# Kernel tuning notes

Hardware: AMD Instinct MI355X
Metric: run time of the kernel (lower is better)

The kernel has to match this reference:

```python
import jax, jax.numpy as jnp
import numpy as np

TOP_K = 2
EPS = 1e-10


def setup_inputs() -> dict:
    key = jax.random.key(0)
    k1, k2, k3, k4 = jax.random.split(key, 4)
    B, S, H, E = 4, 2048, 1024, 8
    tokens = jax.random.normal(k1, (B, S, H), dtype=jnp.float32)
    router_w = jax.random.normal(k2, (E, H), dtype=jnp.float32) * (1.0 / np.sqrt(H))
    router_b = jax.random.normal(k3, (E,), dtype=jnp.float32) * 0.01
    expert_weights = jax.random.normal(k4, (E, H, H), dtype=jnp.float32) * (1.0 / np.sqrt(H))
    return {"tokens": tokens, "router_w": router_w, "router_b": router_b,
            "expert_weights": expert_weights}


def reference(tokens, router_w, router_b, expert_weights):
    B, S, H = tokens.shape
    E = expert_weights.shape[0]
    # Router (torch Linear: x @ W^T + b)
    logits = jnp.einsum('bsh,eh->bse', tokens, router_w) + router_b  # [B,S,E]
    probs = jax.nn.softmax(logits, axis=-1)
    top_p, top_i = jax.lax.top_k(probs, TOP_K)            # [B,S,K]
    w = top_p / (jnp.sum(top_p, axis=-1, keepdims=True) + EPS)  # normalized weights

    x = tokens.reshape(-1, H)                              # [N,H]
    idx = top_i.reshape(-1, TOP_K)                         # [N,K]
    wf = w.reshape(-1, TOP_K)                              # [N,K]

    # Expert GEMM: compute all experts then gather selected (dense, vectorized
    # equivalent of the sort/pad/grouped-GEMM dispatch; padded rows with
    # original_indices==-1 never contribute to the output).
    y_all = jnp.einsum('nh,ehd->ned', x, expert_weights)   # [N,E,H]
    y_k = jnp.take_along_axis(y_all, idx[:, :, None], axis=1)  # [N,K,H]

    out = jnp.einsum('nk,nkh->nh', wf, y_k)                # weighted combine
    acc = jnp.clip(jnp.sum(wf, axis=-1), EPS, None)        # weight accumulator
    out = (out / acc[:, None]).reshape(B, S, H)

    # epsilon scale tying output to normalized router probs (gradient path)
    scale = 1.0 + jnp.sum(w, axis=-1, keepdims=True) * EPS  # [B,S,1]
    return out * scale
```

## Files before the change

### kernel.cpp

```cpp
#include <hip/hip_runtime.h>
#include <stdint.h>

#define N_TOK 8192
#define H_DIM 1024
#define N_EXP 8
#define GEMM_GRID 1024

typedef __bf16 bf16x8 __attribute__((ext_vector_type(8)));
typedef float floatx4 __attribute__((ext_vector_type(4)));

typedef __attribute__((address_space(1))) void GV;
typedef __attribute__((address_space(3))) void LV;

static __device__ __forceinline__ unsigned short f2b(float f) {
    union { float f; unsigned int i; } v; v.f = f;
    unsigned int u = v.i;
    return (unsigned short)((u + 0x7FFFu + ((u >> 16) & 1u)) >> 16);
}
static __device__ __forceinline__ float b2f(unsigned short u) {
    union { unsigned int i; float f; } v; v.i = ((unsigned int)u) << 16; return v.f;
}

__global__ __launch_bounds__(256) void k_front(
    const float* __restrict__ tokens,
    const float* __restrict__ router_w,
    const float* __restrict__ router_b,
    const float* __restrict__ W,
    float* __restrict__ w_arr,
    unsigned short* __restrict__ tokb,
    unsigned short* __restrict__ Bp,
    int* __restrict__ cnt, int* __restrict__ bucket)
{
    const int t = threadIdx.x;

    if (blockIdx.x >= 1024) {
        const int idx = blockIdx.x - 1024;
        const int kg = idx & 127;
        const int e  = idx >> 7;
        const int d  = t * 4;
        const float* src = W + ((size_t)e * H_DIM + kg * 8) * H_DIM + d;
        float col[8][4];
#pragma unroll
        for (int j = 0; j < 8; ++j) {
            float4 v = *(const float4*)(src + (size_t)j * H_DIM);
            col[j][0] = v.x; col[j][1] = v.y; col[j][2] = v.z; col[j][3] = v.w;
        }
        unsigned short* dst = Bp + ((size_t)(e * 128 + kg) * H_DIM + d) * 8;
#pragma unroll
        for (int k = 0; k < 4; ++k) {
            unsigned short v[8];
#pragma unroll
            for (int j = 0; j < 8; ++j) v[j] = f2b(col[j][k]);
            *(uint4*)(dst + (size_t)k * 8) = *(uint4*)v;
        }
        return;
    }

    __shared__ int bcnt[N_EXP];
    __shared__ int blist[N_EXP][16];
    if (t < N_EXP) bcnt[t] = 0;
    __syncthreads();

    const int wv = t >> 6, lane = t & 63;
    const int n0 = blockIdx.x * 8 + wv * 2;

    float x0[16], x1[16];
    const float* xp0 = tokens + (size_t)n0 * H_DIM + lane * 16;
    const float* xp1 = xp0 + H_DIM;
#pragma unroll
    for (int i = 0; i < 4; ++i) {
        float4 v = *(const float4*)(xp0 + i * 4);
        x0[i * 4 + 0] = v.x; x0[i * 4 + 1] = v.y; x0[i * 4 + 2] = v.z; x0[i * 4 + 3] = v.w;
        float4 u = *(const float4*)(xp1 + i * 4);
        x1[i * 4 + 0] = u.x; x1[i * 4 + 1] = u.y; x1[i * 4 + 2] = u.z; x1[i * 4 + 3] = u.w;
    }
    {
        unsigned short xb[16];
#pragma unroll
        for (int j = 0; j < 16; ++j) xb[j] = f2b(x0[j]);
        unsigned short* dp = tokb + (size_t)n0 * H_DIM + lane * 16;
        *(uint4*)(dp) = *(uint4*)(xb); *(uint4*)(dp + 8) = *(uint4*)(xb + 8);
#pragma unroll
        for (int j = 0; j < 16; ++j) xb[j] = f2b(x1[j]);
        dp += H_DIM;
        *(uint4*)(dp) = *(uint4*)(xb); *(uint4*)(dp + 8) = *(uint4*)(xb + 8);
    }

    float a0[N_EXP], a1[N_EXP];
#pragma unroll
    for (int e = 0; e < N_EXP; ++e) {
        const float* wp = router_w + e * H_DIM + lane * 16;
        float s0 = 0.f, s1 = 0.f;
#pragma unroll
        for (int i = 0; i < 4; ++i) {
            float4 v = *(const float4*)(wp + i * 4);
            s0 += x0[i * 4 + 0] * v.x + x0[i * 4 + 1] * v.y + x0[i * 4 + 2] * v.z + x0[i * 4 + 3] * v.w;
            s1 += x1[i * 4 + 0] * v.x + x1[i * 4 + 1] * v.y + x1[i * 4 + 2] * v.z + x1[i * 4 + 3] * v.w;
        }
        a0[e] = s0; a1[e] = s1;
    }
#pragma unroll
    for (int e = 0; e < N_EXP; ++e) {
        float p = a0[e], q = a1[e];
#pragma unroll
        for (int off = 32; off > 0; off >>= 1) { p += __shfl_xor(p, off); q += __shfl_xor(q, off); }
        a0[e] = p; a1[e] = q;
    }

    if (lane == 0) {
#pragma unroll
        for (int k = 0; k < 2; ++k) {
            const int n = n0 + k;
            float lg[N_EXP];
#pragma unroll
            for (int e = 0; e < N_EXP; ++e) lg[e] = (k ? a1[e] : a0[e]) + router_b[e];
            int e0 = 0;
#pragma unroll
            for (int e = 1; e < N_EXP; ++e) if (lg[e] > lg[e0]) e0 = e;
            int e1 = -1;
#pragma unroll
            for (int e = 0; e < N_EXP; ++e) {
                if (e == e0) continue;
                if (e1 < 0 || lg[e] > lg[e1]) e1 = e;
            }
            float w0 = 1.f / (1.f + __expf(lg[e1] - lg[e0]));
            w_arr[n * 2] = w0;
            w_arr[n * 2 + 1] = 1.f - w0;
            int s0 = atomicAdd(&bcnt[e0], 1); blist[e0][s0] = 2 * n;
            int s1 = atomicAdd(&bcnt[e1], 1); blist[e1][s1] = 2 * n + 1;
        }
    }
    __syncthreads();

    if (t < N_EXP) {
        int c = bcnt[t];
        if (c > 0) {
            int base = atomicAdd(&cnt[t], c);
            int* dst = bucket + t * N_TOK + base;
            for (int i = 0; i < c; ++i) dst[i] = blist[t][i];
        }
    }
}

__global__ __launch_bounds__(256, 4) void k_gemm(
    const unsigned short* __restrict__ tokb,
    const unsigned short* __restrict__ Bp,
    const int* __restrict__ cnt, const int* __restrict__ bucket,
    unsigned short* __restrict__ Y)
{
    __shared__ __align__(16) unsigned short Asm[128 * 64];
    __shared__ __align__(16) unsigned short Bsm[8 * 128 * 8];
    __shared__ int rows[128];

    const int t = threadIdx.x;
    const int wv = t >> 6, lane = t & 63;
    const int w_row = wv >> 1, w_col = wv & 1;
    const int m_lane = lane & 15, quad = lane >> 4;
    const int r7 = m_lane & 7;
    const int p_sw = (lane & 7) ^ ((lane >> 3) & 7);

    int cs[N_EXP];
#pragma unroll
    for (int ee = 0; ee < N_EXP; ++ee) cs[ee] = cnt[ee];
    int T = 0;
#pragma unroll
    for (int ee = 0; ee < N_EXP; ++ee) T += (cs[ee] + 127) >> 7;

    const int x = blockIdx.x & 7;
    const int sblk = blockIdx.x >> 3;
    const int q = T >> 3, r = T & 7;
    const int tstart = (x < r) ? x * (q + 1) : r * (q + 1) + (x - r) * q;
    const int tcnt   = (x < r) ? (q + 1) : q;
    const int nloc   = tcnt * 8;

    for (int l = sblk; l < nloc; l += 128) {
        const int tile = tstart + (l >> 3);
        const int nt   = l & 7;
        int base = 0, e = 0, mt = 0;
#pragma unroll
        for (int ee = 0; ee < N_EXP; ++ee) {
            int te = (cs[ee] + 127) >> 7;
            if (tile >= base && tile < base + te) { e = ee; mt = tile - base; }
            base += te;
        }
        const int cnt_local = cs[e] - mt * 128;
        const int d0 = nt * 128;

        __syncthreads();
        if (t < 128)
            rows[t] = (t < cnt_local) ? bucket[e * N_TOK + mt * 128 + t] : -1;
        __syncthreads();

        const unsigned short* aptr[4];
#pragma unroll
        for (int i = 0; i < 4; ++i) {
            int rr = i * 32 + wv * 8 + (lane >> 3);
            int rid = rows[rr];
            int tok = (rid >= 0) ? (rid >> 1) : 0;
            aptr[i] = tokb + (size_t)tok * H_DIM + p_sw * 8;
        }
        const unsigned short* bbase = Bp
            + ((size_t)(e * 128 + (t >> 7)) * H_DIM + d0 + (t & 127)) * 8;

        floatx4 acc[4][4];
#pragma unroll
        for (int i = 0; i < 4; ++i)
#pragma unroll
            for (int j = 0; j < 4; ++j) acc[i][j] = (floatx4){0.f, 0.f, 0.f, 0.f};

        for (int kt = 0; kt < H_DIM / 64; ++kt) {
#pragma unroll
            for (int i = 0; i < 4; ++i) {
                __builtin_amdgcn_global_load_lds(
                    (GV*)(aptr[i] + kt * 64),
                    (LV*)(&Asm[i * 2048 + wv * 512]), 16, 0, 0);
                __builtin_amdgcn_global_load_lds(
                    (GV*)(bbase + (size_t)i * 16384 + (size_t)kt * 65536),
                    (LV*)(&Bsm[i * 2048 + wv * 512]), 16, 0, 0);
            }
            __syncthreads();

#pragma unroll
            for (int s = 0; s < 2; ++s) {
                bf16x8 a[4], b[4];
#pragma unroll
                for (int i = 0; i < 4; ++i) {
                    int row = w_row * 64 + i * 16 + m_lane;
                    a[i] = *(const bf16x8*)&Asm[row * 64 + ((s * 4 + quad) ^ r7) * 8];
                }
#pragma unroll
                for (int j = 0; j < 4; ++j)
                    b[j] = *(const bf16x8*)&Bsm[((s * 4 + quad) * 128 + w_col * 64 + j * 16 + m_lane) * 8];
#pragma unroll
                for (int i = 0; i < 4; ++i)
#pragma unroll
                    for (int j = 0; j < 4; ++j)
                        acc[i][j] = __builtin_amdgcn_mfma_f32_16x16x32_bf16(a[i], b[j], acc[i][j], 0, 0, 0);
            }
            __syncthreads();
        }

#pragma unroll
        for (int i = 0; i < 4; ++i) {
            const int lr_base = w_row * 64 + i * 16 + quad * 4;
#pragma unroll
            for (int reg = 0; reg < 4; ++reg) {
                const int lr = lr_base + reg;
                const int rid = rows[lr];
                if (rid >= 0) {
                    unsigned short v[4];
#pragma unroll
                    for (int j = 0; j < 4; ++j) v[j] = f2b(acc[i][j][reg]);
                    *(uint2*)(Y + (size_t)rid * H_DIM + d0 + w_col * 64 + m_lane * 4) = *(uint2*)v;
                }
            }
        }
    }
}

__global__ __launch_bounds__(256) void k_combine(
    const unsigned short* __restrict__ Y, const float* __restrict__ w_arr,
    float* __restrict__ out)
{
    __shared__ __align__(16) unsigned short Ys[4 * H_DIM];
    const int t = threadIdx.x;
    const int b = blockIdx.x;
    const int wv = t >> 6, lane = t & 63;
    const unsigned short* src = Y + (size_t)b * 4 * H_DIM;
#pragma unroll
    for (int r = 0; r < 2; ++r) {
        __builtin_amdgcn_global_load_lds(
            (GV*)(src + (size_t)r * 2048 + wv * 512 + lane * 8),
            (LV*)(&Ys[r * 2048 + wv * 512]), 16, 0, 0);
    }
    __syncthreads();

    const int tok = t >> 7;
    const int n = 2 * b + tok;
    const int d0 = (t & 127) * 8;
    const int seg = d0 >> 7;
    const int dseg = d0 & 127;
    const int wc = dseg >> 6;
    const int j  = (dseg >> 4) & 3;
    const int m0 = dseg & 15;
    const int sbase = tok * 2 * H_DIM + seg * 128 + wc * 64 + j;
    const float w0 = w_arr[2 * n], w1 = w_arr[2 * n + 1];

    float o[8];
#pragma unroll
    for (int k = 0; k < 8; ++k) {
        int s = sbase + (m0 + k) * 4;
        o[k] = w0 * b2f(Ys[s]) + w1 * b2f(Ys[s + H_DIM]);
    }
    float4* op = (float4*)(out + (size_t)n * H_DIM + d0);
    op[0] = make_float4(o[0], o[1], o[2], o[3]);
    op[1] = make_float4(o[4], o[5], o[6], o[7]);
}

extern "C" void kernel_launch(void* const* d_in, const int* in_sizes, int n_in,
                              void* d_out, int out_size, void* d_ws, size_t ws_size,
                              hipStream_t stream)
{
    const float* tokens   = (const float*)d_in[0];
    const float* router_w = (const float*)d_in[1];
    const float* router_b = (const float*)d_in[2];
    const float* W        = (const float*)d_in[3];
    float* out = (float*)d_out;

    char* ws = (char*)d_ws;
    int*   cnt    = (int*)(ws);
    float* w_arr  = (float*)(ws + 34816);
    int*   bucket = (int*)(ws + 100352);
    unsigned short* tokb = (unsigned short*)(ws + 362496);
    unsigned short* Bp   = (unsigned short*)(ws + 17139712);
    unsigned short* Y    = (unsigned short*)(ws + 33916928);

    hipMemsetAsync(cnt, 0, N_EXP * sizeof(int), stream);
    k_front  <<<2048, 256, 0, stream>>>(tokens, router_w, router_b, W,
                                        w_arr, tokb, Bp, cnt, bucket);
    k_gemm   <<<GEMM_GRID, 256, 0, stream>>>(tokb, Bp, cnt, bucket, Y);
    k_combine<<<N_TOK * (H_DIM / 8) / 256, 256, 0, stream>>>(Y, w_arr, out);
}
```

Baseline: 178.6 us.

## Split-K the leftover GEMM tiles across idle blocks with an fp32 partial-sum fix-up

The grouped GEMM splits the leftover M-tiles of each XCD group (those beyond the 16 tiles per group) across four K-quarters. These quarters run on blocks that would otherwise take a second full tile, which is meant to even out the tail imbalance. Each block writes fp32 partials to a workspace buffer, and a new k_fix kernel sums the four partials, converts to bf16 and scatters the rows into Y. This adds an extra kernel launch and extra partial-sum memory traffic. Split mode is only used when the workspace is large enough, and its mapping assumes there are exactly 16 or 17 tiles per group.

```diff
diff --git a/kernel.cpp b/kernel.cpp
--- a/kernel.cpp
+++ b/kernel.cpp
@@ -146,7 +146,7 @@
     const unsigned short* __restrict__ tokb,
     const unsigned short* __restrict__ Bp,
     const int* __restrict__ cnt, const int* __restrict__ bucket,
-    unsigned short* __restrict__ Y)
+    unsigned short* __restrict__ Y, float* __restrict__ Yp, int split_ok)
 {
     __shared__ __align__(16) unsigned short Asm[128 * 64];
     __shared__ __align__(16) unsigned short Bsm[8 * 128 * 8];
@@ -173,9 +173,39 @@
     const int tcnt   = (x < r) ? (q + 1) : q;
     const int nloc   = tcnt * 8;
 
-    for (int l = sblk; l < nloc; l += 128) {
-        const int tile = tstart + (l >> 3);
-        const int nt   = l & 7;
+    int t0_tile, t0_nt, t0_k0, t0_k1, t0_os;
+    int t1_tile = -1, t1_nt = 0, t1_k0 = 0, t1_k1 = 0, t1_os = -1;
+    if (split_ok) {
+        if (x < r && sblk < 32) {
+            const int oi = sblk >> 2, qk = sblk & 3;
+            t0_tile = tstart + 16; t0_nt = oi;
+            t0_k0 = qk * 4; t0_k1 = qk * 4 + 4;
+            t0_os = (x * 8 + oi) * 4 + qk;
+            t1_tile = tstart + (sblk >> 3); t1_nt = sblk & 7;
+            t1_k0 = 0; t1_k1 = 16; t1_os = -1;
+        } else {
+            t0_tile = tstart + (sblk >> 3); t0_nt = sblk & 7;
+            t0_k0 = 0; t0_k1 = 16; t0_os = -1;
+        }
+    } else {
+        t0_tile = tstart + (sblk >> 3); t0_nt = sblk & 7;
+        t0_k0 = 0; t0_k1 = 16; t0_os = -1;
+        if (sblk + 128 < nloc) {
+            const int l2 = sblk + 128;
+            t1_tile = tstart + (l2 >> 3); t1_nt = l2 & 7;
+            t1_k0 = 0; t1_k1 = 16; t1_os = -1;
+        }
+    }
+
+#pragma unroll 2
+    for (int tk = 0; tk < 2; ++tk) {
+        const int tile = tk ? t1_tile : t0_tile;
+        if (tile < 0) continue;
+        const int nt = tk ? t1_nt : t0_nt;
+        const int k0 = tk ? t1_k0 : t0_k0;
+        const int k1 = tk ? t1_k1 : t0_k1;
+        const int os = tk ? t1_os : t0_os;
+
         int base = 0, e = 0, mt = 0;
 #pragma unroll
         for (int ee = 0; ee < N_EXP; ++ee) {
@@ -208,7 +238,7 @@
 #pragma unroll
             for (int j = 0; j < 4; ++j) acc[i][j] = (floatx4){0.f, 0.f, 0.f, 0.f};
 
-        for (int kt = 0; kt < H_DIM / 64; ++kt) {
+        for (int kt = k0; kt < k1; ++kt) {
 #pragma unroll
             for (int i = 0; i < 4; ++i) {
                 __builtin_amdgcn_global_load_lds(
@@ -240,21 +270,87 @@
             __syncthreads();
         }
 
-#pragma unroll
-        for (int i = 0; i < 4; ++i) {
-            const int lr_base = w_row * 64 + i * 16 + quad * 4;
-#pragma unroll
-            for (int reg = 0; reg < 4; ++reg) {
-                const int lr = lr_base + reg;
-                const int rid = rows[lr];
-                if (rid >= 0) {
-                    unsigned short v[4];
-#pragma unroll
-                    for (int j = 0; j < 4; ++j) v[j] = f2b(acc[i][j][reg]);
-                    *(uint2*)(Y + (size_t)rid * H_DIM + d0 + w_col * 64 + m_lane * 4) = *(uint2*)v;
+        if (os < 0) {
+#pragma unroll
+            for (int i = 0; i < 4; ++i) {
+                const int lr_base = w_row * 64 + i * 16 + quad * 4;
+#pragma unroll
+                for (int reg = 0; reg < 4; ++reg) {
+                    const int lr = lr_base + reg;
+                    const int rid = rows[lr];
+                    if (rid >= 0) {
+                        unsigned short v[4];
+#pragma unroll
+                        for (int j = 0; j < 4; ++j) v[j] = f2b(acc[i][j][reg]);
+                        *(uint2*)(Y + (size_t)rid * H_DIM + d0 + w_col * 64 + m_lane * 4) = *(uint2*)v;
+                    }
                 }
             }
-        }
+        } else {
+            float* dst = Yp + (size_t)os * 16384;
+#pragma unroll
+            for (int i = 0; i < 4; ++i) {
+#pragma unroll
+                for (int reg = 0; reg < 4; ++reg) {
+                    const int lr = w_row * 64 + i * 16 + quad * 4 + reg;
+                    float4 v = make_float4(acc[i][0][reg], acc[i][1][reg],
+                                           acc[i][2][reg], acc[i][3][reg]);
+                    *(float4*)(dst + lr * 128 + w_col * 64 + m_lane * 4) = v;
+                }
+            }
+        }
+    }
+}
+
+__global__ __launch_bounds__(256) void k_fix(
+    const int* __restrict__ cnt, const int* __restrict__ bucket,
+    const float* __restrict__ Yp, unsigned short* __restrict__ Y)
+{
+    int cs[N_EXP];
+#pragma unroll
+    for (int ee = 0; ee < N_EXP; ++ee) cs[ee] = cnt[ee];
+    int T = 0;
+#pragma unroll
+    for (int ee = 0; ee < N_EXP; ++ee) T += (cs[ee] + 127) >> 7;
+    const int q = T >> 3, r = T & 7;
+    const int o = blockIdx.x;
+    if (o >= 8 * r) return;
+    const int x = o >> 3, oi = o & 7;
+    const int tile = x * (q + 1) + q;
+    const int nt = oi;
+
+    int base = 0, e = 0, mt = 0;
+#pragma unroll
+    for (int ee = 0; ee < N_EXP; ++ee) {
+        int te = (cs[ee] + 127) >> 7;
+        if (tile >= base && tile < base + te) { e = ee; mt = tile - base; }
+        base += te;
+    }
+    const int cnt_local = cs[e] - mt * 128;
+    const int d0 = nt * 128;
+
+    const int t = threadIdx.x;
+    const int lr = t >> 1, half = t & 1;
+    const int rid = (lr < cnt_local) ? bucket[e * N_TOK + mt * 128 + lr] : -1;
+    if (rid < 0) return;
+
+    const float* s = Yp + (size_t)o * 4 * 16384 + lr * 128 + half * 64;
+    unsigned short* dst = Y + (size_t)rid * H_DIM + d0 + half * 64;
+#pragma unroll
+    for (int c = 0; c < 64; c += 8) {
+        float sum[8];
+#pragma unroll
+        for (int k = 0; k < 8; ++k) sum[k] = s[c + k];
+#pragma unroll
+        for (int qk = 1; qk < 4; ++qk) {
+            const float* sq = s + qk * 16384;
+#pragma unroll
+            for (int k = 0; k < 8; ++k) sum[k] += sq[c + k];
+        }
+        unsigned short v[8];
+#pragma unroll
+        for (int k = 0; k < 8; ++k) v[k] = f2b(sum[k]);
+        *(uint4*)(dst + c) = *(uint4*)v;
     }
 }
 
@@ -314,10 +410,15 @@
     unsigned short* tokb = (unsigned short*)(ws + 362496);
     unsigned short* Bp   = (unsigned short*)(ws + 17139712);
     unsigned short* Y    = (unsigned short*)(ws + 33916928);
+    float* Yp = (float*)(ws + 67471360);
+
+    const int split_ok = (ws_size >= 82151424ull) ? 1 : 0;
 
     hipMemsetAsync(cnt, 0, N_EXP * sizeof(int), stream);
     k_front  <<<2048, 256, 0, stream>>>(tokens, router_w, router_b, W,
                                         w_arr, tokb, Bp, cnt, bucket);
-    k_gemm   <<<GEMM_GRID, 256, 0, stream>>>(tokb, Bp, cnt, bucket, Y);
+    k_gemm   <<<GEMM_GRID, 256, 0, stream>>>(tokb, Bp, cnt, bucket, Y, Yp, split_ok);
+    if (split_ok)
+        k_fix<<<56, 256, 0, stream>>>(cnt, bucket, Yp, Y);
     k_combine<<<N_TOK * (H_DIM / 8) / 256, 256, 0, stream>>>(Y, w_arr, out);
 }
```

Result: slower. 190.0 us (+6.4%).

## Fuse weighted combine into expert GEMM epilogue with atomic adds, split-K tail tiles

Applied to the files above, without the earlier changes.

Removes the combine kernel and the bf16 intermediate Y buffer. The GEMM epilogue now scales each result by its routing weight and atomically adds it into a zeroed fp32 output. The tile schedule is rewritten so the leftover remainder tile is split along K into four pieces, which balances work across blocks; this relies on the same atomic accumulation. The cost is a full memset of the output and roughly 16M scalar float atomics. The schedule also assumes a fixed tile count per group (at most 17 tiles, 128 blocks per group), which holds for this input size.

```diff
diff --git a/kernel.cpp b/kernel.cpp
--- a/kernel.cpp
+++ b/kernel.cpp
@@ -16,9 +16,6 @@
     union { float f; unsigned int i; } v; v.f = f;
     unsigned int u = v.i;
     return (unsigned short)((u + 0x7FFFu + ((u >> 16) & 1u)) >> 16);
-}
-static __device__ __forceinline__ float b2f(unsigned short u) {
-    union { unsigned int i; float f; } v; v.i = ((unsigned int)u) << 16; return v.f;
 }
 
 __global__ __launch_bounds__(256) void k_front(
@@ -146,7 +143,7 @@
     const unsigned short* __restrict__ tokb,
     const unsigned short* __restrict__ Bp,
     const int* __restrict__ cnt, const int* __restrict__ bucket,
-    unsigned short* __restrict__ Y)
+    const float* __restrict__ w_arr, float* __restrict__ out)
 {
     __shared__ __align__(16) unsigned short Asm[128 * 64];
     __shared__ __align__(16) unsigned short Bsm[8 * 128 * 8];
@@ -170,12 +167,28 @@
     const int sblk = blockIdx.x >> 3;
     const int q = T >> 3, r = T & 7;
     const int tstart = (x < r) ? x * (q + 1) : r * (q + 1) + (x - r) * q;
-    const int tcnt   = (x < r) ? (q + 1) : q;
-    const int nloc   = tcnt * 8;
-
-    for (int l = sblk; l < nloc; l += 128) {
-        const int tile = tstart + (l >> 3);
-        const int nt   = l & 7;
+
+    int t0_tile, t0_nt, t0_k0, t0_k1;
+    int t1_tile = -1, t1_nt = 0, t1_k0 = 0, t1_k1 = 0;
+    if (x < r && sblk < 32) {
+        const int oi = sblk >> 2, qk = sblk & 3;
+        t0_tile = tstart + 16; t0_nt = oi;
+        t0_k0 = qk * 4; t0_k1 = qk * 4 + 4;
+        t1_tile = tstart + (sblk >> 3); t1_nt = sblk & 7;
+        t1_k0 = 0; t1_k1 = 16;
+    } else {
+        t0_tile = tstart + (sblk >> 3); t0_nt = sblk & 7;
+        t0_k0 = 0; t0_k1 = 16;
+    }
+
+#pragma unroll 2
+    for (int tk = 0; tk < 2; ++tk) {
+        const int tile = tk ? t1_tile : t0_tile;
+        if (tile < 0) continue;
+        const int nt = tk ? t1_nt : t0_nt;
+        const int k0 = tk ? t1_k0 : t0_k0;
+        const int k1 = tk ? t1_k1 : t0_k1;
+
         int base = 0, e = 0, mt = 0;
 #pragma unroll
         for (int ee = 0; ee < N_EXP; ++ee) {
@@ -208,7 +221,7 @@
 #pragma unroll
             for (int j = 0; j < 4; ++j) acc[i][j] = (floatx4){0.f, 0.f, 0.f, 0.f};
 
-        for (int kt = 0; kt < H_DIM / 64; ++kt) {
+        for (int kt = k0; kt < k1; ++kt) {
 #pragma unroll
             for (int i = 0; i < 4; ++i) {
                 __builtin_amdgcn_global_load_lds(
@@ -248,53 +261,15 @@
                 const int lr = lr_base + reg;
                 const int rid = rows[lr];
                 if (rid >= 0) {
-                    unsigned short v[4];
-#pragma unroll
-                    for (int j = 0; j < 4; ++j) v[j] = f2b(acc[i][j][reg]);
-                    *(uint2*)(Y + (size_t)rid * H_DIM + d0 + w_col * 64 + m_lane * 4) = *(uint2*)v;
+                    const float w = w_arr[rid];
+                    float* orow = out + (size_t)(rid >> 1) * H_DIM + d0 + w_col * 64 + m_lane;
+#pragma unroll
+                    for (int j = 0; j < 4; ++j)
+                        unsafeAtomicAdd(orow + j * 16, w * acc[i][j][reg]);
                 }
             }
         }
     }
-}
-
-__global__ __launch_bounds__(256) void k_combine(
-    const unsigned short* __restrict__ Y, const float* __restrict__ w_arr,
-    float* __restrict__ out)
-{
-    __shared__ __align__(16) unsigned short Ys[4 * H_DIM];
-    const int t = threadIdx.x;
-    const int b = blockIdx.x;
-    const int wv = t >> 6, lane = t & 63;
-    const unsigned short* src = Y + (size_t)b * 4 * H_DIM;
-#pragma unroll
-    for (int r = 0; r < 2; ++r) {
-        __builtin_amdgcn_global_load_lds(
-            (GV*)(src + (size_t)r * 2048 + wv * 512 + lane * 8),
-            (LV*)(&Ys[r * 2048 + wv * 512]), 16, 0, 0);
-    }
-    __syncthreads();
-
-    const int tok = t >> 7;
-    const int n = 2 * b + tok;
-    const int d0 = (t & 127) * 8;
-    const int seg = d0 >> 7;
-    const int dseg = d0 & 127;
-    const int wc = dseg >> 6;
-    const int j  = (dseg >> 4) & 3;
-    const int m0 = dseg & 15;
-    const int sbase = tok * 2 * H_DIM + seg * 128 + wc * 64 + j;
-    const float w0 = w_arr[2 * n], w1 = w_arr[2 * n + 1];
-
-    float o[8];
-#pragma unroll
-    for (int k = 0; k < 8; ++k) {
-        int s = sbase + (m0 + k) * 4;
-        o[k] = w0 * b2f(Ys[s]) + w1 * b2f(Ys[s + H_DIM]);
-    }
-    float4* op = (float4*)(out + (size_t)n * H_DIM + d0);
-    op[0] = make_float4(o[0], o[1], o[2], o[3]);
-    op[1] = make_float4(o[4], o[5], o[6], o[7]);
 }
 
 extern "C" void kernel_launch(void* const* d_in, const int* in_sizes, int n_in,
@@ -313,11 +288,10 @@
     int*   bucket = (int*)(ws + 100352);
     unsigned short* tokb = (unsigned short*)(ws + 362496);
     unsigned short* Bp   = (unsigned short*)(ws + 17139712);
-    unsigned short* Y    = (unsigned short*)(ws + 33916928);
 
     hipMemsetAsync(cnt, 0, N_EXP * sizeof(int), stream);
-    k_front  <<<2048, 256, 0, stream>>>(tokens, router_w, router_b, W,
-                                        w_arr, tokb, Bp, cnt, bucket);
-    k_gemm   <<<GEMM_GRID, 256, 0, stream>>>(tokb, Bp, cnt, bucket, Y);
-    k_combine<<<N_TOK * (H_DIM / 8) / 256, 256, 0, stream>>>(Y, w_arr, out);
-}
+    hipMemsetAsync(out, 0, (size_t)N_TOK * H_DIM * sizeof(float), stream);
+    k_front<<<2048, 256, 0, stream>>>(tokens, router_w, router_b, W,
+                                      w_arr, tokb, Bp, cnt, bucket);
+    k_gemm <<<GEMM_GRID, 256, 0, stream>>>(tokb, Bp, cnt, bucket, w_arr, out);
+}
```

Result: slower. 203.9 us (+14.2%).
